# Kernel optimization log

Hardware: AMD Instinct MI355X
Metric: run time of the kernel (lower is better)

## Reference

```python
import jax, jax.numpy as jnp
import numpy as np

BS, IC, L = 8, 64, 32768
OC, K = 64, 3
STRIDE, PAD, DIL = 1, 1, 1
ALPHA = 0.5  # SmoothQuant scaling_factor
QMAX = 127.0  # symmetric int8 fake quant


def fake_quant(t):
    # per-tensor symmetric int8 fake quantization with straight-through estimator
    amax = jnp.max(jnp.abs(jax.lax.stop_gradient(t)))
    s = jnp.where(amax == 0, 1.0, amax / QMAX)
    q = jnp.clip(jnp.round(t / s), -QMAX, QMAX) * s
    return t + jax.lax.stop_gradient(q - t)


def setup_inputs() -> dict:
    key = jax.random.key(0)
    k1, k2, k3 = jax.random.split(key, 3)
    x = jax.random.normal(k1, (BS, IC, L), dtype=jnp.float32)
    weight = jax.random.normal(k2, (OC, IC, K), dtype=jnp.float32) * 0.05
    bias = jax.random.normal(k3, (OC,), dtype=jnp.float32) * 0.01
    return {"x": x, "weight": weight, "bias": bias}


def reference(x, weight, bias):
    bs, ic, length = x.shape
    out_len = (length + 2 * PAD - DIL * (K - 1) - 1) // STRIDE + 1
    # im2col / unfold: (bs, ic, K, out_len) with F.unfold's channel-major, kernel-pos-minor order
    xp = jnp.pad(x, ((0, 0), (0, 0), (PAD, PAD)))
    patches = jnp.stack(
        [xp[:, :, j * DIL : j * DIL + STRIDE * (out_len - 1) + 1 : STRIDE] for j in range(K)],
        axis=2,
    )  # (bs, ic, K, out_len)
    cols = patches.reshape(bs, ic * K, out_len).transpose(0, 2, 1).reshape(bs * out_len, ic * K)
    w = weight.reshape(OC, ic * K)
    # dynamic SmoothQuant scales (detached in original)
    w_scale = jnp.max(jnp.abs(jax.lax.stop_gradient(w)), axis=0)        # (ic*K,)
    act_scale = jnp.max(jnp.abs(jax.lax.stop_gradient(cols)), axis=0)   # (ic*K,)
    scale = act_scale ** ALPHA / w_scale ** (1.0 - ALPHA)
    scale = jnp.where(scale == 0, 1.0, scale)
    xq = fake_quant(cols / scale)
    wq = fake_quant(w * scale)
    out = xq @ wq.T  # (bs*out_len, OC)
    out = out.reshape(bs, out_len, OC).transpose(0, 2, 1) + bias[None, :, None]
    return out
```

## Files before the change

kernel.cpp:

```cpp
#include <hip/hip_runtime.h>

#define L_LEN 32768
#define QMAXF 127.0f

typedef __attribute__((ext_vector_type(4))) int v4i;


__global__ __launch_bounds__(256) void actamax_kernel(const float* __restrict__ x,
                                                      float* __restrict__ wsf) {
    const int ic = blockIdx.x, b = blockIdx.y;
    const float4* row = (const float4*)(x + ((size_t)(b*64 + ic) << 15));
    float mA = 0.0f, mNF = 0.0f, mNL = 0.0f;
    for (int f = threadIdx.x; f < 8192; f += 256) {
        float4 v = row[f];
        float ax = fabsf(v.x), ay = fabsf(v.y), az = fabsf(v.z), aw = fabsf(v.w);
        float m4 = fmaxf(fmaxf(ax, ay), fmaxf(az, aw));
        mA = fmaxf(mA, m4);
        if (f == 0) {
            mNF = fmaxf(mNF, fmaxf(ay, fmaxf(az, aw)));
            mNL = fmaxf(mNL, m4);
        } else if (f == 8191) {
            mNF = fmaxf(mNF, m4);
            mNL = fmaxf(mNL, fmaxf(ax, fmaxf(ay, az)));
        } else {
            mNF = fmaxf(mNF, m4);
            mNL = fmaxf(mNL, m4);
        }
    }
    #pragma unroll
    for (int off = 32; off; off >>= 1) {
        mA  = fmaxf(mA,  __shfl_down(mA,  off));
        mNF = fmaxf(mNF, __shfl_down(mNF, off));
        mNL = fmaxf(mNL, __shfl_down(mNL, off));
    }
    __shared__ float red[3][4];
    int wid = threadIdx.x >> 6;
    if ((threadIdx.x & 63) == 0) { red[0][wid] = mA; red[1][wid] = mNF; red[2][wid] = mNL; }
    __syncthreads();
    if (threadIdx.x == 0) {
        mA  = fmaxf(fmaxf(red[0][0], red[0][1]), fmaxf(red[0][2], red[0][3]));
        mNF = fmaxf(fmaxf(red[1][0], red[1][1]), fmaxf(red[1][2], red[1][3]));
        mNL = fmaxf(fmaxf(red[2][0], red[2][1]), fmaxf(red[2][2], red[2][3]));
        float* p = wsf + (ic*8 + b)*3;
        p[0] = mNL; p[1] = mA; p[2] = mNF;
    }
}

__global__ __launch_bounds__(256) void prep_kernel(const float* __restrict__ w,
                                                   float* __restrict__ wsf,
                                                   unsigned int* __restrict__ wsa) {
    __shared__ float scl[192];
    __shared__ float red[256];
    const int tid = threadIdx.x;
    float ax = 0.0f, aw = 0.0f;
    if (tid < 192) {
        float wsc = 0.0f;
        #pragma unroll 8
        for (int o = 0; o < 64; ++o) wsc = fmaxf(wsc, fabsf(w[o*192 + tid]));
        int ic = tid / 3, k = tid - ic*3;
        float asc = 0.0f;
        #pragma unroll
        for (int b = 0; b < 8; ++b) asc = fmaxf(asc, wsf[(ic*8 + b)*3 + k]);
        float sc = sqrtf(asc) / sqrtf(wsc);
        if (sc == 0.0f) sc = 1.0f;
        scl[tid] = sc;
        ax = asc / sc;
        aw = wsc * sc;
    }
    red[tid] = ax; __syncthreads();
    for (int s = 128; s; s >>= 1) { if (tid < s) red[tid] = fmaxf(red[tid], red[tid+s]); __syncthreads(); }
    float axm = red[0]; __syncthreads();
    red[tid] = aw; __syncthreads();
    for (int s = 128; s; s >>= 1) { if (tid < s) red[tid] = fmaxf(red[tid], red[tid+s]); __syncthreads(); }
    float awm = red[0];
    float s_x = (axm == 0.0f) ? 1.0f : axm / QMAXF;
    float s_w = (awm == 0.0f) ? 1.0f : awm / QMAXF;
    if (tid < 192) wsf[1536 + tid] = 1.0f / (scl[tid] * s_x);
    if (tid == 0)  wsf[1728] = s_x * s_w;
    __syncthreads();
    for (int idx = tid; idx < 3072; idx += 256) {
        int oc = idx / 48, dwi = idx - oc*48, j0 = dwi*4;
        unsigned pk = 0;
        #pragma unroll
        for (int bb = 0; bb < 4; ++bb) {
            int j = j0 + bb;
            float q = rintf((w[oc*192 + j] * scl[j]) / s_w);
            q = fminf(fmaxf(q, -QMAXF), QMAXF);
            pk |= (((unsigned)(int)q) & 255u) << (8*bb);
        }
        int mt = oc >> 4, m = oc & 15, c = j0 >> 4, s = c >> 2, kq = c & 3;
        wsa[((mt*3 + s)*64 + kq*16 + m)*4 + ((j0 & 15) >> 2)] = pk;
    }
}

__global__ __launch_bounds__(256) void conv_mfma_kernel(const float* __restrict__ x,
                                                        const float* __restrict__ bias,
                                                        const float* __restrict__ wsf,
                                                        const v4i* __restrict__ wsa,
                                                        float* __restrict__ out) {
    __shared__ int bsm[3072];
    const int tid  = threadIdx.x;
    const int b    = blockIdx.y;
    const int t0   = blockIdx.x << 6;
    const int lane = tid & 63;
    const int w    = tid >> 6;

    v4i afrag[12];
    #pragma unroll
    for (int i = 0; i < 12; ++i) afrag[i] = wsa[i*64 + lane];

    const int tq  = tid & 15;
    const int icg = tid >> 4;
    const int tb  = tq << 2;

    float rv[12];
    #pragma unroll
    for (int jj = 0; jj < 12; ++jj) rv[jj] = wsf[1536 + icg*12 + jj];

    float xv[4][6];
    #pragma unroll
    for (int ici = 0; ici < 4; ++ici) {
        const float* row = x + (((size_t)(b*64 + icg*4 + ici)) << 15) + t0 + tb;
        float4 mid = *(const float4*)row;
        float lm = (t0 + tb > 0)           ? row[-1] : 0.0f;
        float rp = (t0 + tb + 4 < L_LEN)   ? row[4]  : 0.0f;
        xv[ici][0] = lm;   xv[ici][1] = mid.x; xv[ici][2] = mid.y;
        xv[ici][3] = mid.z; xv[ici][4] = mid.w; xv[ici][5] = rp;
    }

    #pragma unroll
    for (int dt = 0; dt < 4; ++dt) {
        int t  = tb + dt;
        int wt = t >> 4, n = t & 15;
        #pragma unroll
        for (int dw = 0; dw < 3; ++dw) {
            unsigned pk = 0;
            #pragma unroll
            for (int bb = 0; bb < 4; ++bb) {
                int jloc = dw*4 + bb;
                int ici = jloc / 3, k = jloc - ici*3;
                float q = rintf(xv[ici][dt + k] * rv[jloc]);
                q = fminf(fmaxf(q, -QMAXF), QMAXF);
                pk |= (((unsigned)(int)q) & 255u) << (8*bb);
            }
            int j0 = icg*12 + dw*4;
            int c = j0 >> 4, s = c >> 2, kq = c & 3;
            bsm[((wt*3 + s)*64 + kq*16 + n)*4 + ((j0 & 15) >> 2)] = (int)pk;
        }
    }
    __syncthreads();

    v4i acc[4];
    #pragma unroll
    for (int mt = 0; mt < 4; ++mt) acc[mt] = (v4i){0,0,0,0};
    const v4i* bsmv = (const v4i*)bsm;
    #pragma unroll
    for (int s = 0; s < 3; ++s) {
        v4i bf = bsmv[(w*3 + s)*64 + lane];
        #pragma unroll
        for (int mt = 0; mt < 4; ++mt)
            acc[mt] = __builtin_amdgcn_mfma_i32_16x16x64_i8(afrag[mt*3 + s], bf, acc[mt], 0, 0, 0);
    }

    const float sxw = wsf[1728];
    const int tg   = t0 + (w << 4) + (lane & 15);
    const int rowq = (lane >> 4) << 2;
    #pragma unroll
    for (int mt = 0; mt < 4; ++mt) {
        #pragma unroll
        for (int i = 0; i < 4; ++i) {
            int oc = mt*16 + rowq + i;
            out[(((size_t)(b*64 + oc)) << 15) + tg] = (float)acc[mt][i] * sxw + bias[oc];
        }
    }
}

extern "C" void kernel_launch(void* const* d_in, const int* in_sizes, int n_in,
                              void* d_out, int out_size, void* d_ws, size_t ws_size,
                              hipStream_t stream) {
    const float* x    = (const float*)d_in[0];
    const float* w    = (const float*)d_in[1];
    const float* bias = (const float*)d_in[2];
    float* out = (float*)d_out;
    float* wsf = (float*)d_ws;
    unsigned int* wsa = (unsigned int*)((char*)d_ws + 8192);

    hipLaunchKernelGGL(actamax_kernel,  dim3(64, 8),  dim3(256), 0, stream, x, wsf);
    hipLaunchKernelGGL(prep_kernel,     dim3(1),      dim3(256), 0, stream, w, wsf, wsa);
    hipLaunchKernelGGL(conv_mfma_kernel,dim3(512, 8), dim3(256), 0, stream, x, bias, wsf, (const v4i*)wsa, out);
}
```

Measured before the change: 167.3 us.

## Fuse prep into conv kernel, loop several tiles per block, widen amax blocks

The separate single-block prep kernel is removed. Every conv block now redundantly recomputes the SmoothQuant scales and the quantized weight fragments in shared memory, which removes one launch and the serialization behind a one-block kernel. Each conv block processes four 64-wide time tiles, prefetching the next tile's inputs before the MFMA work to amortize the prologue. The amax kernel uses 1024-thread blocks with an unrolled loop. In exchange, each of 1024 blocks repeats the weight max over 12K floats and two block reductions, and the grid has fewer blocks.

```diff
diff --git a/kernel.cpp b/kernel.cpp
--- a/kernel.cpp
+++ b/kernel.cpp
@@ -2,16 +2,19 @@
 
 #define L_LEN 32768
 #define QMAXF 127.0f
+#define TPB 4
 
 typedef __attribute__((ext_vector_type(4))) int v4i;
 
 
-__global__ __launch_bounds__(256) void actamax_kernel(const float* __restrict__ x,
-                                                      float* __restrict__ wsf) {
+__global__ __launch_bounds__(1024) void actamax_kernel(const float* __restrict__ x,
+                                                       float* __restrict__ wsf) {
     const int ic = blockIdx.x, b = blockIdx.y;
     const float4* row = (const float4*)(x + ((size_t)(b*64 + ic) << 15));
     float mA = 0.0f, mNF = 0.0f, mNL = 0.0f;
-    for (int f = threadIdx.x; f < 8192; f += 256) {
+    #pragma unroll
+    for (int i = 0; i < 8; ++i) {
+        int f = threadIdx.x + (i << 10);
         float4 v = row[f];
         float ax = fabsf(v.x), ay = fabsf(v.y), az = fabsf(v.z), aw = fabsf(v.w);
         float m4 = fmaxf(fmaxf(ax, ay), fmaxf(az, aw));
@@ -33,26 +36,39 @@
         mNF = fmaxf(mNF, __shfl_down(mNF, off));
         mNL = fmaxf(mNL, __shfl_down(mNL, off));
     }
-    __shared__ float red[3][4];
+    __shared__ float red[3][16];
     int wid = threadIdx.x >> 6;
     if ((threadIdx.x & 63) == 0) { red[0][wid] = mA; red[1][wid] = mNF; red[2][wid] = mNL; }
     __syncthreads();
     if (threadIdx.x == 0) {
-        mA  = fmaxf(fmaxf(red[0][0], red[0][1]), fmaxf(red[0][2], red[0][3]));
-        mNF = fmaxf(fmaxf(red[1][0], red[1][1]), fmaxf(red[1][2], red[1][3]));
-        mNL = fmaxf(fmaxf(red[2][0], red[2][1]), fmaxf(red[2][2], red[2][3]));
+        mA = red[0][0]; mNF = red[1][0]; mNL = red[2][0];
+        #pragma unroll
+        for (int i = 1; i < 16; ++i) {
+            mA  = fmaxf(mA,  red[0][i]);
+            mNF = fmaxf(mNF, red[1][i]);
+            mNL = fmaxf(mNL, red[2][i]);
+        }
         float* p = wsf + (ic*8 + b)*3;
         p[0] = mNL; p[1] = mA; p[2] = mNF;
     }
 }
 
-__global__ __launch_bounds__(256) void prep_kernel(const float* __restrict__ w,
-                                                   float* __restrict__ wsf,
-                                                   unsigned int* __restrict__ wsa) {
+__global__ __launch_bounds__(256) void fused_conv_kernel(const float* __restrict__ x,
+                                                         const float* __restrict__ w,
+                                                         const float* __restrict__ bias,
+                                                         const float* __restrict__ wsf,
+                                                         float* __restrict__ out) {
+    __shared__ int   bsm[3072];
     __shared__ float scl[192];
     __shared__ float red[256];
-    const int tid = threadIdx.x;
-    float ax = 0.0f, aw = 0.0f;
+    __shared__ float bias_s[64];
+
+    const int tid  = threadIdx.x;
+    const int b    = blockIdx.y;
+    const int lane = tid & 63;
+    const int wv   = tid >> 6;
+
+    float ax = 0.0f, aww = 0.0f;
     if (tid < 192) {
         float wsc = 0.0f;
         #pragma unroll 8
@@ -60,24 +76,24 @@
         int ic = tid / 3, k = tid - ic*3;
         float asc = 0.0f;
         #pragma unroll
-        for (int b = 0; b < 8; ++b) asc = fmaxf(asc, wsf[(ic*8 + b)*3 + k]);
+        for (int bb = 0; bb < 8; ++bb) asc = fmaxf(asc, wsf[(ic*8 + bb)*3 + k]);
         float sc = sqrtf(asc) / sqrtf(wsc);
         if (sc == 0.0f) sc = 1.0f;
         scl[tid] = sc;
-        ax = asc / sc;
-        aw = wsc * sc;
-    }
+        ax  = asc / sc;
+        aww = wsc * sc;
+    }
+    if (tid < 64) bias_s[tid] = bias[tid];
     red[tid] = ax; __syncthreads();
     for (int s = 128; s; s >>= 1) { if (tid < s) red[tid] = fmaxf(red[tid], red[tid+s]); __syncthreads(); }
     float axm = red[0]; __syncthreads();
-    red[tid] = aw; __syncthreads();
+    red[tid] = aww; __syncthreads();
     for (int s = 128; s; s >>= 1) { if (tid < s) red[tid] = fmaxf(red[tid], red[tid+s]); __syncthreads(); }
     float awm = red[0];
-    float s_x = (axm == 0.0f) ? 1.0f : axm / QMAXF;
-    float s_w = (awm == 0.0f) ? 1.0f : awm / QMAXF;
-    if (tid < 192) wsf[1536 + tid] = 1.0f / (scl[tid] * s_x);
-    if (tid == 0)  wsf[1728] = s_x * s_w;
-    __syncthreads();
+    const float s_x = (axm == 0.0f) ? 1.0f : axm / QMAXF;
+    const float s_w = (awm == 0.0f) ? 1.0f : awm / QMAXF;
+    const float sxw = s_x * s_w;
+
     for (int idx = tid; idx < 3072; idx += 256) {
         int oc = idx / 48, dwi = idx - oc*48, j0 = dwi*4;
         unsigned pk = 0;
@@ -89,25 +105,13 @@
             pk |= (((unsigned)(int)q) & 255u) << (8*bb);
         }
         int mt = oc >> 4, m = oc & 15, c = j0 >> 4, s = c >> 2, kq = c & 3;
-        wsa[((mt*3 + s)*64 + kq*16 + m)*4 + ((j0 & 15) >> 2)] = pk;
-    }
-}
-
-__global__ __launch_bounds__(256) void conv_mfma_kernel(const float* __restrict__ x,
-                                                        const float* __restrict__ bias,
-                                                        const float* __restrict__ wsf,
-                                                        const v4i* __restrict__ wsa,
-                                                        float* __restrict__ out) {
-    __shared__ int bsm[3072];
-    const int tid  = threadIdx.x;
-    const int b    = blockIdx.y;
-    const int t0   = blockIdx.x << 6;
-    const int lane = tid & 63;
-    const int w    = tid >> 6;
-
+        bsm[((mt*3 + s)*64 + kq*16 + m)*4 + ((j0 & 15) >> 2)] = (int)pk;
+    }
+    __syncthreads();
     v4i afrag[12];
-    #pragma unroll
-    for (int i = 0; i < 12; ++i) afrag[i] = wsa[i*64 + lane];
+    const v4i* bsmv = (const v4i*)bsm;
+    #pragma unroll
+    for (int i = 0; i < 12; ++i) afrag[i] = bsmv[i*64 + lane];
 
     const int tq  = tid & 15;
     const int icg = tid >> 4;
@@ -115,62 +119,90 @@
 
     float rv[12];
     #pragma unroll
-    for (int jj = 0; jj < 12; ++jj) rv[jj] = wsf[1536 + icg*12 + jj];
+    for (int jj = 0; jj < 12; ++jj) rv[jj] = 1.0f / (scl[icg*12 + jj] * s_x);
 
     float xv[4][6];
-    #pragma unroll
-    for (int ici = 0; ici < 4; ++ici) {
-        const float* row = x + (((size_t)(b*64 + icg*4 + ici)) << 15) + t0 + tb;
-        float4 mid = *(const float4*)row;
-        float lm = (t0 + tb > 0)           ? row[-1] : 0.0f;
-        float rp = (t0 + tb + 4 < L_LEN)   ? row[4]  : 0.0f;
-        xv[ici][0] = lm;   xv[ici][1] = mid.x; xv[ici][2] = mid.y;
-        xv[ici][3] = mid.z; xv[ici][4] = mid.w; xv[ici][5] = rp;
-    }
-
-    #pragma unroll
-    for (int dt = 0; dt < 4; ++dt) {
-        int t  = tb + dt;
-        int wt = t >> 4, n = t & 15;
-        #pragma unroll
-        for (int dw = 0; dw < 3; ++dw) {
-            unsigned pk = 0;
-            #pragma unroll
-            for (int bb = 0; bb < 4; ++bb) {
-                int jloc = dw*4 + bb;
-                int ici = jloc / 3, k = jloc - ici*3;
-                float q = rintf(xv[ici][dt + k] * rv[jloc]);
-                q = fminf(fmaxf(q, -QMAXF), QMAXF);
-                pk |= (((unsigned)(int)q) & 255u) << (8*bb);
-            }
-            int j0 = icg*12 + dw*4;
-            int c = j0 >> 4, s = c >> 2, kq = c & 3;
-            bsm[((wt*3 + s)*64 + kq*16 + n)*4 + ((j0 & 15) >> 2)] = (int)pk;
-        }
-    }
-    __syncthreads();
-
-    v4i acc[4];
-    #pragma unroll
-    for (int mt = 0; mt < 4; ++mt) acc[mt] = (v4i){0,0,0,0};
-    const v4i* bsmv = (const v4i*)bsm;
-    #pragma unroll
-    for (int s = 0; s < 3; ++s) {
-        v4i bf = bsmv[(w*3 + s)*64 + lane];
-        #pragma unroll
-        for (int mt = 0; mt < 4; ++mt)
-            acc[mt] = __builtin_amdgcn_mfma_i32_16x16x64_i8(afrag[mt*3 + s], bf, acc[mt], 0, 0, 0);
-    }
-
-    const float sxw = wsf[1728];
-    const int tg   = t0 + (w << 4) + (lane & 15);
-    const int rowq = (lane >> 4) << 2;
-    #pragma unroll
-    for (int mt = 0; mt < 4; ++mt) {
-        #pragma unroll
-        for (int i = 0; i < 4; ++i) {
-            int oc = mt*16 + rowq + i;
-            out[(((size_t)(b*64 + oc)) << 15) + tg] = (float)acc[mt][i] * sxw + bias[oc];
+    {
+        const int t0 = (blockIdx.x * TPB) << 6;
+        #pragma unroll
+        for (int ici = 0; ici < 4; ++ici) {
+            const float* rowp = x + (((size_t)(b*64 + icg*4 + ici)) << 15) + t0 + tb;
+            float4 mid = *(const float4*)rowp;
+            float lm = (t0 + tb > 0)           ? rowp[-1] : 0.0f;
+            float rp = (t0 + tb + 4 < L_LEN)   ? rowp[4]  : 0.0f;
+            xv[ici][0] = lm;    xv[ici][1] = mid.x; xv[ici][2] = mid.y;
+            xv[ici][3] = mid.z; xv[ici][4] = mid.w; xv[ici][5] = rp;
+        }
+    }
+
+    for (int it = 0; it < TPB; ++it) {
+        const int t0c = (blockIdx.x * TPB + it) << 6;
+
+        unsigned pkq[12];
+        #pragma unroll
+        for (int dt = 0; dt < 4; ++dt) {
+            #pragma unroll
+            for (int dw = 0; dw < 3; ++dw) {
+                unsigned pk = 0;
+                #pragma unroll
+                for (int bb = 0; bb < 4; ++bb) {
+                    int jloc = dw*4 + bb;
+                    int ici = jloc / 3, k = jloc - ici*3;
+                    float q = rintf(xv[ici][dt + k] * rv[jloc]);
+                    q = fminf(fmaxf(q, -QMAXF), QMAXF);
+                    pk |= (((unsigned)(int)q) & 255u) << (8*bb);
+                }
+                pkq[dt*3 + dw] = pk;
+            }
+        }
+
+        __syncthreads();
+        #pragma unroll
+        for (int dt = 0; dt < 4; ++dt) {
+            int t = tb + dt, wt = t >> 4, n = t & 15;
+            #pragma unroll
+            for (int dw = 0; dw < 3; ++dw) {
+                int j0 = icg*12 + dw*4;
+                int c = j0 >> 4, s = c >> 2, kq = c & 3;
+                bsm[((wt*3 + s)*64 + kq*16 + n)*4 + ((j0 & 15) >> 2)] = (int)pkq[dt*3 + dw];
+            }
+        }
+        __syncthreads();
+
+        if (it + 1 < TPB) {
+            const int t0n = (blockIdx.x * TPB + it + 1) << 6;
+            #pragma unroll
+            for (int ici = 0; ici < 4; ++ici) {
+                const float* rowp = x + (((size_t)(b*64 + icg*4 + ici)) << 15) + t0n + tb;
+                float4 mid = *(const float4*)rowp;
+                float lm = (t0n + tb > 0)          ? rowp[-1] : 0.0f;
+                float rp = (t0n + tb + 4 < L_LEN)  ? rowp[4]  : 0.0f;
+                xv[ici][0] = lm;    xv[ici][1] = mid.x; xv[ici][2] = mid.y;
+                xv[ici][3] = mid.z; xv[ici][4] = mid.w; xv[ici][5] = rp;
+            }
+        }
+
+        v4i acc[4];
+        #pragma unroll
+        for (int mt = 0; mt < 4; ++mt) acc[mt] = (v4i){0,0,0,0};
+        const v4i* bsmv2 = (const v4i*)bsm;
+        #pragma unroll
+        for (int s = 0; s < 3; ++s) {
+            v4i bf = bsmv2[(wv*3 + s)*64 + lane];
+            #pragma unroll
+            for (int mt = 0; mt < 4; ++mt)
+                acc[mt] = __builtin_amdgcn_mfma_i32_16x16x64_i8(afrag[mt*3 + s], bf, acc[mt], 0, 0, 0);
+        }
+
+        const int tg   = t0c + (wv << 4) + (lane & 15);
+        const int rowq = (lane >> 4) << 2;
+        #pragma unroll
+        for (int mt = 0; mt < 4; ++mt) {
+            #pragma unroll
+            for (int i = 0; i < 4; ++i) {
+                int oc = mt*16 + rowq + i;
+                out[(((size_t)(b*64 + oc)) << 15) + tg] = (float)acc[mt][i] * sxw + bias_s[oc];
+            }
         }
     }
 }
@@ -183,9 +215,8 @@
     const float* bias = (const float*)d_in[2];
     float* out = (float*)d_out;
     float* wsf = (float*)d_ws;
-    unsigned int* wsa = (unsigned int*)((char*)d_ws + 8192);
-
-    hipLaunchKernelGGL(actamax_kernel,  dim3(64, 8),  dim3(256), 0, stream, x, wsf);
-    hipLaunchKernelGGL(prep_kernel,     dim3(1),      dim3(256), 0, stream, w, wsf, wsa);
-    hipLaunchKernelGGL(conv_mfma_kernel,dim3(512, 8), dim3(256), 0, stream, x, bias, wsf, (const v4i*)wsa, out);
+
+    hipLaunchKernelGGL(actamax_kernel,   dim3(64, 8),  dim3(1024), 0, stream, x, wsf);
+    hipLaunchKernelGGL(fused_conv_kernel, dim3(512 / TPB, 8), dim3(256), 0, stream,
+                       x, w, bias, wsf, out);
 }
```

Measured after the change: 165.1 us. About the same (-1.3%).
